# Kernel tuning notes

Measured on AMD Instinct MI355X. Metric: run time of the kernel, lower is better.

The kernel has to match this reference:

```python
import jax, jax.numpy as jnp
import numpy as np

N = 100000
F_IN = 512
HID = 256
C = 64
E = 3200000
K = 5


def _gcn_conv(h, W, b, src, dst, n):
    # h: [n, f_in] -> [n, f_out]; symmetric-normalized GCN with self-loops.
    hw = h @ W  # [n, f_out]
    loop = jnp.arange(n)
    s = jnp.concatenate([src, loop])
    d = jnp.concatenate([dst, loop])
    deg = jax.ops.segment_sum(jnp.ones_like(d, dtype=hw.dtype), d, num_segments=n)
    dinv = jnp.where(deg > 0, jax.lax.rsqrt(deg), 0.0)
    norm = dinv[s] * dinv[d]  # [E+n]
    out = jax.ops.segment_sum(norm[:, None] * hw[s], d, num_segments=n)
    return out + b


def _conv1d(x, w, b):
    # x: [1, C_in, L], w: [C_out, C_in, K], SAME padding (pad = (K-1)/2)
    y = jax.lax.conv_general_dilated(x, w, window_strides=(1,), padding='SAME',
                                     dimension_numbers=('NCW', 'OIW', 'NCW'))
    return y + b[None, :, None]


def setup_inputs() -> dict:
    key = jax.random.key(0)
    ks = jax.random.split(key, 16)

    def glorot(k, shape):
        fan_in, fan_out = shape[-2], shape[-1]
        lim = np.sqrt(6.0 / (fan_in + fan_out))
        return jax.random.uniform(k, shape, jnp.float32, -lim, lim)

    x = jax.random.normal(ks[0], (N, F_IN), jnp.float32)
    edge_index = jax.random.randint(ks[1], (2, E), 0, N, dtype=jnp.int64)

    W1 = glorot(ks[2], (F_IN, HID));  b1 = jnp.zeros((HID,), jnp.float32)
    W2 = glorot(ks[3], (HID, C));     b2 = jnp.zeros((C,), jnp.float32)
    Wp = glorot(ks[4], (C, 1));       bp = jnp.zeros((1,), jnp.float32)
    s1 = 1.0 / np.sqrt(C * K)
    cw1 = jax.random.uniform(ks[5], (C, C, K), jnp.float32, -s1, s1)
    cb1 = jax.random.uniform(ks[6], (C,), jnp.float32, -s1, s1)
    cw2 = jax.random.uniform(ks[7], (C, C, K), jnp.float32, -s1, s1)
    cb2 = jax.random.uniform(ks[8], (C,), jnp.float32, -s1, s1)
    Wl = glorot(ks[9], (2 * C, C));   bl = jnp.zeros((C,), jnp.float32)

    return {"x": x, "edge_index": edge_index, "W1": W1, "b1": b1, "W2": W2,
            "b2": b2, "Wp": Wp, "bp": bp, "cw1": cw1, "cb1": cb1,
            "cw2": cw2, "cb2": cb2, "Wl": Wl, "bl": bl}


def reference(x, edge_index, W1, b1, W2, b2, Wp, bp, cw1, cb1, cw2, cb2, Wl, bl):
    src, dst = edge_index[0], edge_index[1]
    n = x.shape[0]
    h = jax.nn.relu(_gcn_conv(x, W1, b1, src, dst, n))      # [N, HID]
    x1 = _gcn_conv(h, W2, b2, src, dst, n)                   # [N, C]

    g_score = x1 @ Wp + bp                                   # [N, 1]
    sort_idx = jnp.argsort(g_score[:, 0])                    # [N]
    inverse_idx = jnp.argsort(sort_idx)                      # [N]
    g_sorted = g_score[sort_idx]                             # [N, 1]
    sorted_x = g_sorted * x1[sort_idx]                       # [N, C]

    sx = sorted_x.T[None]                                    # [1, C, N]
    sx = jax.nn.relu(_conv1d(sx, cw1, cb1))
    sx = _conv1d(sx, cw2, cb2)
    sorted_out = sx[0].T                                     # [N, C]
    x2 = sorted_out[inverse_idx]                             # [N, C]

    out = jnp.concatenate([x1, x2], axis=1) @ Wl + bl        # [N, C]
    return jax.nn.log_softmax(out, axis=1)
```

## Files before the change

kernel.cpp:

```cpp
#include <hip/hip_runtime.h>
#include <cstdint>
#include <cstddef>

#define NF_IN 512
#define NHID 256
#define NC 64

typedef _Float16 f16x8 __attribute__((ext_vector_type(8)));
typedef float f32x4 __attribute__((ext_vector_type(4)));


__global__ void kb_hist(const int* __restrict__ dst, int e_total,
                        int* __restrict__ gh, int nbk){
  __shared__ int h[512];
  int t = threadIdx.x;
  for (int i=t;i<nbk;i+=256) h[i]=0;
  __syncthreads();
  int e0 = blockIdx.x*4096;
  #pragma unroll
  for (int j=0;j<16;j++){
    int e = e0 + j*256 + t;
    if (e < e_total) atomicAdd(&h[dst[e]>>8], 1);
  }
  __syncthreads();
  for (int i=t;i<nbk;i+=256) if (h[i]) atomicAdd(&gh[i], h[i]);
}

__global__ void k_scan1(int* __restrict__ data, int n){
  __shared__ int P[256];
  int t = threadIdx.x;
  int chunk = (n + 255) >> 8;
  int base = t*chunk;
  int s = 0;
  for (int j=0;j<chunk;j++) if (base+j<n) s += data[base+j];
  P[t]=s; __syncthreads();
  for (int o=1;o<256;o<<=1){
    int v = (t>=o)? P[t-o]:0; __syncthreads();
    P[t]+=v; __syncthreads();
  }
  int run = (t>0)? P[t-1] : 0;
  for (int j=0;j<chunk;j++) if (base+j<n){ int v = data[base+j]; data[base+j]=run; run+=v; }
}

__global__ void kb_copy(const int* __restrict__ a, int* __restrict__ b, int m){
  int i = blockIdx.x*256 + threadIdx.x;
  if (i < m) b[i] = a[i];
}

__global__ void kb_scatter(const int* __restrict__ src, const int* __restrict__ dst,
                           int e_total, int* __restrict__ bcur,
                           unsigned* __restrict__ pairs, int nbk){
  __shared__ int h[512];
  __shared__ int cb[512];
  int t = threadIdx.x;
  for (int i=t;i<nbk;i+=256) h[i]=0;
  __syncthreads();
  int e0 = blockIdx.x*4096;
  int d[16], s_[16];
  #pragma unroll
  for (int j=0;j<16;j++){
    int e = e0 + j*256 + t;
    if (e < e_total){ d[j]=dst[e]; s_[j]=src[e]; atomicAdd(&h[d[j]>>8],1); }
    else d[j] = -1;
  }
  __syncthreads();
  for (int i=t;i<nbk;i+=256){
    int c = h[i];
    cb[i] = c ? atomicAdd(&bcur[i], c) : 0;
    h[i] = 0;
  }
  __syncthreads();
  #pragma unroll
  for (int j=0;j<16;j++){
    if (d[j] >= 0){
      int bkt = d[j]>>8;
      int pos = cb[bkt] + atomicAdd(&h[bkt],1);
      pairs[pos] = ((unsigned)(d[j]&255)<<24) | (unsigned)s_[j];
    }
  }
}

__global__ __launch_bounds__(256) void kb_build(const unsigned* __restrict__ pairs,
    const int* __restrict__ bbase, int e_total, int nbk, int n,
    int* __restrict__ rowptr, int* __restrict__ cnt, float* __restrict__ dinv,
    int* __restrict__ csr){
  __shared__ int cL[256];
  __shared__ int sc[256];
  __shared__ int rpL[256];
  int b = blockIdx.x, t = threadIdx.x;
  int beg = bbase[b];
  int end = (b == nbk-1) ? e_total : bbase[b+1];
  cL[t] = 0; __syncthreads();
  for (int i=beg+t; i<end; i+=256) atomicAdd(&cL[pairs[i]>>24], 1);
  __syncthreads();
  int v = cL[t]; sc[t] = v; __syncthreads();
  for (int o=1;o<256;o<<=1){
    int w = (t>=o)? sc[t-o]:0; __syncthreads();
    sc[t] += w; __syncthreads();
  }
  rpL[t] = sc[t] - v;
  int node = b*256 + t;
  if (node < n){
    rowptr[node] = beg + rpL[t];
    cnt[node]    = v;
    dinv[node]   = 1.0f / sqrtf((float)(v + 1));
  }
  cL[t] = 0; __syncthreads();
  for (int i=beg+t; i<end; i+=256){
    unsigned p = pairs[i];
    int loc = p >> 24;
    int pos = beg + rpL[loc] + atomicAdd(&cL[loc], 1);
    csr[pos] = (int)(p & 0xFFFFFFu);
  }
}

__global__ __launch_bounds__(256) void k_sortnb(int* __restrict__ csr,
    const int* __restrict__ rowptr, const int* __restrict__ cnt, int n){
  int node = blockIdx.x*4 + (threadIdx.x>>6);
  int lane = threadIdx.x & 63;
  if (node >= n) return;
  int beg = rowptr[node], num = cnt[node];
  if (num <= 1 || num > 64) return;
  int v = (lane < num) ? csr[beg+lane] : 0x7fffffff;
  #pragma unroll
  for (int k=2; k<=64; k<<=1){
    for (int j=k>>1; j>0; j>>=1){
      int p = __shfl_xor(v, j);
      bool dirUp = ((lane & k) == 0);
      bool lower = ((lane & j) == 0);
      int mn = (v < p) ? v : p;
      int mx = (v < p) ? p : v;
      v = (dirUp == lower) ? mn : mx;
    }
  }
  if (lane < num) csr[beg+lane] = v;
}

__global__ void k_wsplit(const float* __restrict__ W, _Float16* __restrict__ WhT,
                         _Float16* __restrict__ WlT){
  int idx = blockIdx.x*256 + threadIdx.x;
  if (idx < NF_IN*NHID){
    int k = idx >> 8, nn = idx & 255;
    float w = W[idx];
    _Float16 h = (_Float16)w;
    _Float16 l = (_Float16)((w - (float)h) * 2048.0f);
    WhT[(size_t)nn*NF_IN + k] = h;
    WlT[(size_t)nn*NF_IN + k] = l;
  }
}

__global__ __launch_bounds__(512, 2) void k_mgemm1(
    const float* __restrict__ A, int lda,
    const _Float16* __restrict__ BhT, const _Float16* __restrict__ BlT, int ldb,
    float* __restrict__ C, int ldc, int M, int K, const float* __restrict__ dinv){
  __shared__ __align__(16) _Float16 Ah[128*40];
  __shared__ __align__(16) _Float16 Al[128*40];
  __shared__ __align__(16) _Float16 Bh[256*40];
  __shared__ __align__(16) _Float16 Bl[256*40];
  int t = threadIdx.x;
  int m0 = blockIdx.x*128;
  int wave = t>>6, lane = t&63;
  int wm = (wave>>2)*64, wn = (wave&3)*64;

  int arow = t>>2, akb = (t&3)*8;
  int ga = m0 + arow; if (ga >= M) ga = M - 1;
  const float* aptr = A + (size_t)ga*lda + akb;
  int brow = t>>1, bkb = (t&1)*16;
  const _Float16* bhp = BhT + (size_t)brow*ldb + bkb;
  const _Float16* blp = BlT + (size_t)brow*ldb + bkb;

  float4 a0 = *(const float4*)(aptr);
  float4 a1 = *(const float4*)(aptr+4);
  f16x8  b0 = *(const f16x8*)(bhp);
  f16x8  b1 = *(const f16x8*)(bhp+8);
  f16x8  c0 = *(const f16x8*)(blp);
  f16x8  c1 = *(const f16x8*)(blp+8);

  f32x4 acc1[4][4] = {};
  f32x4 acc2[4][4] = {};

  for (int k0 = 0; k0 < K; k0 += 32){
    __syncthreads();
    {
      float av[8] = {a0.x,a0.y,a0.z,a0.w, a1.x,a1.y,a1.z,a1.w};
      f16x8 h0, l0;
      #pragma unroll
      for (int j=0;j<8;j++){
        _Float16 hh = (_Float16)av[j];
        h0[j] = hh;
        l0[j] = (_Float16)((av[j] - (float)hh) * 2048.0f);
      }
      *(f16x8*)&Ah[arow*40+akb] = h0;
      *(f16x8*)&Al[arow*40+akb] = l0;
      *(f16x8*)&Bh[brow*40+bkb]   = b0;
      *(f16x8*)&Bh[brow*40+bkb+8] = b1;
      *(f16x8*)&Bl[brow*40+bkb]   = c0;
      *(f16x8*)&Bl[brow*40+bkb+8] = c1;
    }
    __syncthreads();
    if (k0 + 32 < K){
      a0 = *(const float4*)(aptr + k0+32);
      a1 = *(const float4*)(aptr + k0+36);
      b0 = *(const f16x8*)(bhp + k0+32);
      b1 = *(const f16x8*)(bhp + k0+40);
      c0 = *(const f16x8*)(blp + k0+32);
      c1 = *(const f16x8*)(blp + k0+40);
    }
    int fr = lane & 15, fk = (lane>>4)*8;
    f16x8 afh[4], afl[4];
    #pragma unroll
    for (int mf=0; mf<4; mf++){
      afh[mf] = *(const f16x8*)&Ah[(wm + mf*16 + fr)*40 + fk];
      afl[mf] = *(const f16x8*)&Al[(wm + mf*16 + fr)*40 + fk];
    }
    #pragma unroll
    for (int nf=0; nf<4; nf++){
      f16x8 bfh = *(const f16x8*)&Bh[(wn + nf*16 + fr)*40 + fk];
      f16x8 bfl = *(const f16x8*)&Bl[(wn + nf*16 + fr)*40 + fk];
      #pragma unroll
      for (int mf=0; mf<4; mf++){
        acc1[mf][nf] = __builtin_amdgcn_mfma_f32_16x16x32_f16(afh[mf], bfh, acc1[mf][nf], 0, 0, 0);
        acc2[mf][nf] = __builtin_amdgcn_mfma_f32_16x16x32_f16(afh[mf], bfl, acc2[mf][nf], 0, 0, 0);
        acc2[mf][nf] = __builtin_amdgcn_mfma_f32_16x16x32_f16(afl[mf], bfh, acc2[mf][nf], 0, 0, 0);
      }
    }
  }

  int fr = lane & 15, fq = lane >> 4;
  #pragma unroll
  for (int mf=0; mf<4; mf++){
    #pragma unroll
    for (int i=0;i<4;i++){
      int row = m0 + wm + mf*16 + fq*4 + i;
      if (row < M){
        float sc = dinv ? dinv[row] : 1.0f;
        #pragma unroll
        for (int nf=0; nf<4; nf++){
          float v = (acc1[mf][nf][i] + 0.00048828125f*acc2[mf][nf][i]) * sc;
          C[(size_t)row*ldc + wn + nf*16 + fr] = v;
        }
      }
    }
  }
}

__global__ __launch_bounds__(256) void k_gemm(const float* __restrict__ A, int lda,
    const float* __restrict__ B, int ldb, float* __restrict__ C, int ldc,
    int M, int K, const float* __restrict__ dinv){
  __shared__ float As[16*68];
  __shared__ float Bs[16*64];
  int t = threadIdx.x;
  int m0 = blockIdx.x*64, n0 = blockIdx.y*64;
  int tx = t & 15, ty = t >> 4;
  float acc[4][4] = {};
  int arow = m0 + (t>>2); if (arow >= M) arow = M-1;
  const float* aptr = A + (size_t)arow*lda + (t&3)*4;
  const float* bptr = B + (size_t)(t>>4)*ldb + n0 + (t&15)*4;
  for (int k0=0; k0<K; k0+=16){
    float4 av = *(const float4*)(aptr + k0);
    float4 bv = *(const float4*)(bptr + (size_t)k0*ldb);
    __syncthreads();
    int ak = (t&3)*4, ar = t>>2;
    As[(ak+0)*68 + ar] = av.x;
    As[(ak+1)*68 + ar] = av.y;
    As[(ak+2)*68 + ar] = av.z;
    As[(ak+3)*68 + ar] = av.w;
    *(float4*)&Bs[(t>>4)*64 + (t&15)*4] = bv;
    __syncthreads();
    #pragma unroll
    for (int kk=0;kk<16;kk++){
      float4 a4 = *(const float4*)&As[kk*68 + (ty<<2)];
      float4 b4 = *(const float4*)&Bs[(kk<<6) + (tx<<2)];
      float aa[4] = {a4.x,a4.y,a4.z,a4.w};
      float bb[4] = {b4.x,b4.y,b4.z,b4.w};
      #pragma unroll
      for (int i=0;i<4;i++)
        #pragma unroll
        for (int j=0;j<4;j++) acc[i][j] += aa[i]*bb[j];
    }
  }
  #pragma unroll
  for (int i=0;i<4;i++){
    int row = m0 + (ty<<2) + i;
    if (row < M){
      float sc = dinv ? dinv[row] : 1.0f;
      float4 vv; vv.x=acc[i][0]*sc; vv.y=acc[i][1]*sc; vv.z=acc[i][2]*sc; vv.w=acc[i][3]*sc;
      *(float4*)&C[(size_t)row*ldc + n0 + (tx<<2)] = vv;
    }
  }
}

__global__ __launch_bounds__(256, 4) void k_agg1(const float* __restrict__ u,
    const int* __restrict__ rowptr, const int* __restrict__ cnt,
    const int* __restrict__ csr, const float* __restrict__ dinv,
    const float* __restrict__ bias, float* __restrict__ outp, int n){
  int wid = blockIdx.x*4 + (threadIdx.x>>6);
  int lane = threadIdx.x & 63;
  if (wid >= n) return;
  const float4* up = (const float4*)u;
  float4 a = up[(size_t)wid*64 + lane];
  float ax=a.x, ay=a.y, az=a.z, aw=a.w;
  int beg = rowptr[wid], num = cnt[wid];
  int e = 0;
  int nb = num >> 4;
  if (nb > 0){
    int my = csr[beg + (lane & 15)];
    float4 v[8], w[8];
    #pragma unroll
    for (int q=0;q<8;q++){ int s = __shfl(my, q); v[q] = up[(size_t)s*64 + lane]; }
    int b = 0;
    for (;;){
      #pragma unroll
      for (int q=0;q<8;q++){ int s = __shfl(my, q+8); w[q] = up[(size_t)s*64 + lane]; }
      #pragma unroll
      for (int q=0;q<8;q++){ ax+=v[q].x; ay+=v[q].y; az+=v[q].z; aw+=v[q].w; }
      b++;
      if (b >= nb){
        #pragma unroll
        for (int q=0;q<8;q++){ ax+=w[q].x; ay+=w[q].y; az+=w[q].z; aw+=w[q].w; }
        break;
      }
      my = csr[beg + b*16 + (lane & 15)];
      #pragma unroll
      for (int q=0;q<8;q++){ int s = __shfl(my, q); v[q] = up[(size_t)s*64 + lane]; }
      #pragma unroll
      for (int q=0;q<8;q++){ ax+=w[q].x; ay+=w[q].y; az+=w[q].z; aw+=w[q].w; }
    }
    e = nb*16;
  }
  for (; e+4 <= num; e+=4){
    int my = csr[beg + e + (lane & 3)];
    float4 v[4];
    #pragma unroll
    for (int q=0;q<4;q++){ int s = __shfl(my, q); v[q] = up[(size_t)s*64 + lane]; }
    #pragma unroll
    for (int q=0;q<4;q++){ ax+=v[q].x; ay+=v[q].y; az+=v[q].z; aw+=v[q].w; }
  }
  for (; e<num; e++){
    int sN = csr[beg+e];
    float4 v = up[(size_t)sN*64 + lane];
    ax+=v.x; ay+=v.y; az+=v.z; aw+=v.w;
  }
  float di = dinv[wid];
  float4 b = ((const float4*)bias)[lane];
  float4 r;
  r.x = fmaxf(di*ax + b.x, 0.f);
  r.y = fmaxf(di*ay + b.y, 0.f);
  r.z = fmaxf(di*az + b.z, 0.f);
  r.w = fmaxf(di*aw + b.w, 0.f);
  ((float4*)outp)[(size_t)wid*64 + lane] = r;
}

__global__ __launch_bounds__(256) void k_agg2g(const float* __restrict__ u,
    const int* __restrict__ rowptr, const int* __restrict__ cnt,
    const int* __restrict__ csr, const float* __restrict__ dinv,
    const float* __restrict__ bias, float* __restrict__ outp, int n,
    const float* __restrict__ Wp, const float* __restrict__ bp,
    float* __restrict__ g, unsigned* __restrict__ keys, unsigned* __restrict__ vals){
  int wid = blockIdx.x*4 + (threadIdx.x>>6);
  int lane = threadIdx.x & 63;
  if (wid >= n) return;
  float acc = u[(size_t)wid*64 + lane];
  int beg = rowptr[wid], num = cnt[wid];
  int e = 0;
  for (; e+16 <= num; e+=16){
    int my = csr[beg + e + (lane & 15)];
    float v[16];
    #pragma unroll
    for (int q=0;q<16;q++){ int s = __shfl(my, q); v[q] = u[(size_t)s*64 + lane]; }
    #pragma unroll
    for (int q=0;q<16;q++) acc += v[q];
  }
  for (; e+4 <= num; e+=4){
    int my = csr[beg + e + (lane & 3)];
    float v[4];
    #pragma unroll
    for (int q=0;q<4;q++){ int s = __shfl(my, q); v[q] = u[(size_t)s*64 + lane]; }
    #pragma unroll
    for (int q=0;q<4;q++) acc += v[q];
  }
  for (; e<num; e++){
    int sN = csr[beg+e];
    acc += u[(size_t)sN*64 + lane];
  }
  float val = dinv[wid]*acc + bias[lane];
  outp[(size_t)wid*64 + lane] = val;
  float wv = val * Wp[lane];
  for (int o=32;o>0;o>>=1) wv += __shfl_xor(wv, o);
  if (lane == 0){
    float gg = wv + bp[0];
    g[wid] = gg;
    unsigned u_ = __float_as_uint(gg);
    u_ = (u_>>31) ? ~u_ : (u_ | 0x80000000u);
    keys[wid] = u_; vals[wid] = (unsigned)wid;
  }
}

__global__ void k_rhist(const unsigned* __restrict__ keys, int shift,
                        int* __restrict__ ghist, int n){
  __shared__ int h[16];
  int t = threadIdx.x;
  if (t < 16) h[t] = 0;
  __syncthreads();
  int base = blockIdx.x*1024 + t*4;
  #pragma unroll
  for (int j=0;j<4;j++)
    if (base+j < n){ int d = (keys[base+j]>>shift)&15; atomicAdd(&h[d],1); }
  __syncthreads();
  if (t < 16) ghist[t*gridDim.x + blockIdx.x] = h[t];
}

__global__ void k_rscatter(const unsigned* __restrict__ keys, const unsigned* __restrict__ vals,
                           int shift, const int* __restrict__ gbase,
                           unsigned* __restrict__ okeys, unsigned* __restrict__ ovals, int n){
  __shared__ int F[16*256];
  __shared__ int P[256];
  int t = threadIdx.x;
  int base = blockIdx.x*1024 + t*4;
  unsigned k[4]; int d[4];
  #pragma unroll
  for (int j=0;j<4;j++){
    bool ok = (base+j < n);
    k[j] = ok ? keys[base+j] : 0u;
    d[j] = (int)((k[j]>>shift)&15u);
    if (!ok) d[j] = -1;
  }
  #pragma unroll
  for (int dig=0;dig<16;dig++){
    int c = 0;
    #pragma unroll
    for (int j=0;j<4;j++) if (d[j]==dig) c++;
    F[dig*256 + t] = c;
  }
  __syncthreads();
  int loc[16]; int s = 0;
  #pragma unroll
  for (int q=0;q<16;q++){ loc[q] = F[t*16+q]; s += loc[q]; }
  P[t] = s; __syncthreads();
  for (int o=1;o<256;o<<=1){
    int v = (t>=o)? P[t-o]:0; __syncthreads();
    P[t] += v; __syncthreads();
  }
  int run = (t>0)? P[t-1] : 0;
  #pragma unroll
  for (int q=0;q<16;q++){ F[t*16+q] = run; run += loc[q]; }
  __syncthreads();
  #pragma unroll
  for (int j=0;j<4;j++){
    if (base+j < n){
      int dd = d[j];
      int r = 0;
      #pragma unroll
      for (int jj=0;jj<4;jj++) if (jj<j && d[jj]==dd) r++;
      int pos = gbase[dd*gridDim.x + blockIdx.x] + (F[dd*256 + t] - F[dd*256]) + r;
      okeys[pos] = k[j];
      ovals[pos] = vals[base+j];
    }
  }
}

__global__ void k_ssx(const unsigned* __restrict__ sidx, const float* __restrict__ g,
                      const float* __restrict__ x1, float* __restrict__ ssx,
                      int* __restrict__ inv, int n){
  int idx = blockIdx.x*256 + threadIdx.x;
  if (idx < n*64){
    int p = idx>>6, c = idx&63;
    int j = (int)sidx[p];
    ssx[idx] = g[j] * x1[(size_t)j*64 + c];
    if (c==0) inv[j] = p;
  }
}

__global__ void k_wt(const float* __restrict__ cw1, const float* __restrict__ cw2,
                     float* __restrict__ wT1, float* __restrict__ wT2){
  int idx = blockIdx.x*256 + threadIdx.x;
  if (idx < 2*20480){
    const float* s = (idx < 20480) ? cw1 : cw2;
    float* o = (idx < 20480) ? wT1 : wT2;
    int i = idx % 20480;
    int kk = i % 5, ci = (i/5) % 64, co = i / 320;
    o[((kk<<6)+ci)*64 + co] = s[i];
  }
}

__global__ __launch_bounds__(256) void k_conv(const float* __restrict__ inp,
    const float* __restrict__ wT, const float* __restrict__ bias,
    float* __restrict__ outp, int n, int do_relu){
  __shared__ float xin[132*65];
  int t = threadIdx.x;
  int r0 = blockIdx.x*128;
  for (int idx=t; idx<132*64; idx+=256){
    int r = idx>>6, c = idx&63;
    int gr = r0 + r - 2;
    xin[r*65 + c] = (gr>=0 && gr<n) ? inp[(size_t)gr*64 + c] : 0.f;
  }
  __syncthreads();
  int rg = t & 15, cg = t >> 4;
  float acc[8][4] = {};
  for (int k=0;k<5;k++){
    for (int ci=0;ci<64;ci++){
      float4 w = *(const float4*)&wT[((k<<6)+ci)*64 + (cg<<2)];
      #pragma unroll
      for (int rr=0;rr<8;rr++){
        float xv = xin[(rg + (rr<<4) + k)*65 + ci];
        acc[rr][0] += xv*w.x; acc[rr][1] += xv*w.y;
        acc[rr][2] += xv*w.z; acc[rr][3] += xv*w.w;
      }
    }
  }
  float4 b = ((const float4*)bias)[cg];
  #pragma unroll
  for (int rr=0;rr<8;rr++){
    int row = r0 + rg + (rr<<4);
    if (row < n){
      float4 v;
      v.x = acc[rr][0]+b.x; v.y = acc[rr][1]+b.y; v.z = acc[rr][2]+b.z; v.w = acc[rr][3]+b.w;
      if (do_relu){ v.x=fmaxf(v.x,0.f); v.y=fmaxf(v.y,0.f); v.z=fmaxf(v.z,0.f); v.w=fmaxf(v.w,0.f); }
      *(float4*)&outp[(size_t)row*64 + (cg<<2)] = v;
    }
  }
}

__global__ __launch_bounds__(256) void k_fgemm(const float* __restrict__ x1,
    const float* __restrict__ y2, const int* __restrict__ inv,
    const float* __restrict__ Wl, const float* __restrict__ bl,
    float* __restrict__ outp, int M){
  __shared__ float As[16*68];
  __shared__ float Bs[16*64];
  __shared__ float Pr[64*16];
  __shared__ float Ms[64];
  __shared__ float Ls[64];
  int t = threadIdx.x;
  int m0 = blockIdx.x*64;
  int tx = t & 15, ty = t >> 4;
  float acc[4][4] = {};
  int arow = m0 + (t>>2); if (arow >= M) arow = M-1;
  int acol0 = (t&3)*4;
  int invr = inv[arow];
  const float* bptr = Wl + (size_t)(t>>4)*64 + tx*4;
  for (int k0=0; k0<128; k0+=16){
    int acol = acol0 + k0;
    float4 av = (acol < 64) ? *(const float4*)&x1[(size_t)arow*64 + acol]
                            : *(const float4*)&y2[(size_t)invr*64 + (acol-64)];
    float4 bv = *(const float4*)(bptr + (size_t)k0*64);
    __syncthreads();
    int ak = (t&3)*4, ar = t>>2;
    As[(ak+0)*68 + ar] = av.x;
    As[(ak+1)*68 + ar] = av.y;
    As[(ak+2)*68 + ar] = av.z;
    As[(ak+3)*68 + ar] = av.w;
    *(float4*)&Bs[(t>>4)*64 + (t&15)*4] = bv;
    __syncthreads();
    #pragma unroll
    for (int kk=0;kk<16;kk++){
      float4 a4 = *(const float4*)&As[kk*68 + (ty<<2)];
      float4 b4 = *(const float4*)&Bs[(kk<<6) + (tx<<2)];
      float aa[4] = {a4.x,a4.y,a4.z,a4.w};
      float bb[4] = {b4.x,b4.y,b4.z,b4.w};
      #pragma unroll
      for (int i=0;i<4;i++)
        #pragma unroll
        for (int j=0;j<4;j++) acc[i][j] += aa[i]*bb[j];
    }
  }
  float v[4][4];
  #pragma unroll
  for (int i=0;i<4;i++)
    #pragma unroll
    for (int j=0;j<4;j++) v[i][j] = acc[i][j] + bl[(tx<<2)+j];
  #pragma unroll
  for (int i=0;i<4;i++){
    float pm = fmaxf(fmaxf(v[i][0],v[i][1]), fmaxf(v[i][2],v[i][3]));
    Pr[((ty<<2)+i)*16 + tx] = pm;
  }
  __syncthreads();
  if (t < 64){
    float m = Pr[t*16];
    #pragma unroll
    for (int k=1;k<16;k++) m = fmaxf(m, Pr[t*16+k]);
    Ms[t] = m;
  }
  __syncthreads();
  #pragma unroll
  for (int i=0;i<4;i++){
    float m = Ms[(ty<<2)+i];
    float ps = expf(v[i][0]-m)+expf(v[i][1]-m)+expf(v[i][2]-m)+expf(v[i][3]-m);
    Pr[((ty<<2)+i)*16 + tx] = ps;
  }
  __syncthreads();
  if (t < 64){
    float s = 0.f;
    #pragma unroll
    for (int k=0;k<16;k++) s += Pr[t*16+k];
    Ls[t] = logf(s);
  }
  __syncthreads();
  #pragma unroll
  for (int i=0;i<4;i++){
    int row = m0 + (ty<<2) + i;
    if (row < M){
      float m = Ms[(ty<<2)+i], l = Ls[(ty<<2)+i];
      float4 o;
      o.x = v[i][0]-m-l; o.y = v[i][1]-m-l; o.z = v[i][2]-m-l; o.w = v[i][3]-m-l;
      *(float4*)&outp[(size_t)row*64 + (tx<<2)] = o;
    }
  }
}

extern "C" void kernel_launch(void* const* d_in, const int* in_sizes, int n_in,
                              void* d_out, int out_size, void* d_ws, size_t ws_size,
                              hipStream_t stream) {
  const float* x   = (const float*)d_in[0];
  const int*   ei  = (const int*)d_in[1];
  const float* W1  = (const float*)d_in[2];
  const float* b1  = (const float*)d_in[3];
  const float* W2  = (const float*)d_in[4];
  const float* b2  = (const float*)d_in[5];
  const float* Wp  = (const float*)d_in[6];
  const float* bp  = (const float*)d_in[7];
  const float* cw1 = (const float*)d_in[8];
  const float* cb1 = (const float*)d_in[9];
  const float* cw2 = (const float*)d_in[10];
  const float* cb2 = (const float*)d_in[11];
  const float* Wl  = (const float*)d_in[12];
  const float* bl  = (const float*)d_in[13];
  float* out = (float*)d_out;

  const int n = in_sizes[0] / NF_IN;
  const int e_total = in_sizes[1] / 2;
  const int* srcp = ei;
  const int* dstp = ei + e_total;

  char* ws = (char*)d_ws;
  size_t off = 0;
  auto take = [&](size_t bytes)->char* {
    char* p = ws + off; off = (off + bytes + 255) & ~(size_t)255; return p;
  };
  const int NB  = (n + 1023) / 1024;
  const int NBK = (n + 255) >> 8;
  const int NEB = (e_total + 4095) / 4096;
  int*      cnt    = (int*)     take((size_t)n*4);
  int*      rowptr = (int*)     take((size_t)n*4);
  float*    dinv   = (float*)   take((size_t)n*4);
  float*    g      = (float*)   take((size_t)n*4);
  int*      inv    = (int*)     take((size_t)n*4);
  unsigned* keys0  = (unsigned*)take((size_t)n*4);
  unsigned* vals0  = (unsigned*)take((size_t)n*4);
  unsigned* keys1  = (unsigned*)take((size_t)n*4);
  unsigned* vals1  = (unsigned*)take((size_t)n*4);
  int*      ghist  = (int*)     take((size_t)(16*NB)*4);
  int*      bh     = (int*)     take(512*4);
  int*      bcur   = (int*)     take(512*4);
  int*      csr    = (int*)     take((size_t)e_total*4);
  float*    wT1    = (float*)   take(20480*4);
  float*    wT2    = (float*)   take(20480*4);
  _Float16* w1h    = (_Float16*)take((size_t)NF_IN*NHID*2);
  _Float16* w1l    = (_Float16*)take((size_t)NF_IN*NHID*2);
  float*    bigA   = (float*)   take((size_t)n*256*4);
  float*    bigB   = (float*)   take((size_t)n*256*4);
  unsigned* pairs  = (unsigned*)bigA;
  float* u1  = bigA;
  float* h   = bigB;
  float* u2  = bigA;
  float* x1  = bigA + (size_t)n*64;
  float* ssx = bigA + (size_t)n*128;
  float* y1  = bigA + (size_t)n*192;
  float* y2  = bigB;

  const int nb128 = (n + 127) / 128;
  const int nb64  = (n + 63) / 64;
  const int nbAgg = (n + 3) / 4;

  hipMemsetAsync(bh, 0, (size_t)NBK*4, stream);
  kb_hist<<<NEB, 256, 0, stream>>>(dstp, e_total, bh, NBK);
  k_scan1<<<1, 256, 0, stream>>>(bh, NBK);
  kb_copy<<<(NBK+255)/256, 256, 0, stream>>>(bh, bcur, NBK);
  kb_scatter<<<NEB, 256, 0, stream>>>(srcp, dstp, e_total, bcur, pairs, NBK);
  kb_build<<<NBK, 256, 0, stream>>>(pairs, bh, e_total, NBK, n, rowptr, cnt, dinv, csr);
  k_sortnb<<<nbAgg, 256, 0, stream>>>(csr, rowptr, cnt, n);

  k_wsplit<<<(NF_IN*NHID+255)/256, 256, 0, stream>>>(W1, w1h, w1l);
  k_mgemm1<<<dim3(nb128, 1), 512, 0, stream>>>(x, NF_IN, w1h, w1l, NF_IN, u1, NHID, n, NF_IN, dinv);
  k_agg1<<<nbAgg, 256, 0, stream>>>(u1, rowptr, cnt, csr, dinv, b1, h, n);

  k_gemm<<<dim3(nb64, 1), 256, 0, stream>>>(h, NHID, W2, NC, u2, NC, n, NHID, dinv);
  k_agg2g<<<nbAgg, 256, 0, stream>>>(u2, rowptr, cnt, csr, dinv, b2, x1, n,
                                     Wp, bp, g, keys0, vals0);

  unsigned *ka = keys0, *va = vals0, *kb = keys1, *vb = vals1;
  for (int p = 0; p < 8; p++){
    k_rhist<<<NB, 256, 0, stream>>>(ka, p*4, ghist, n);
    k_scan1<<<1, 256, 0, stream>>>(ghist, 16*NB);
    k_rscatter<<<NB, 256, 0, stream>>>(ka, va, p*4, ghist, kb, vb, n);
    unsigned* tk = ka; ka = kb; kb = tk;
    unsigned* tv = va; va = vb; vb = tv;
  }

  k_ssx<<<(n*64+255)/256, 256, 0, stream>>>(va, g, x1, ssx, inv, n);

  k_wt<<<(2*20480+255)/256, 256, 0, stream>>>(cw1, cw2, wT1, wT2);
  k_conv<<<(n+127)/128, 256, 0, stream>>>(ssx, wT1, cb1, y1, n, 1);
  k_conv<<<(n+127)/128, 256, 0, stream>>>(y1, wT2, cb2, y2, n, 0);

  k_fgemm<<<nb64, 256, 0, stream>>>(x1, y2, inv, Wl, bl, out, n);
}
```

Before: 1.461 ms.

## Switch radix sort to 8-bit digits with ballot ranking and fused next-pass histogram

Replaces the eight 4-bit radix passes with four 8-bit passes. Ranking within a block now uses wave ballots, and each scatter also builds the next pass's histogram with global atomics, so the separate histogram kernels go away. The scan plus copy of the bucket offsets is merged into one kernel. The per-node neighbour bitonic sort is removed, which changes CSR neighbour order and therefore the floating-point summation order. In exchange, the single-block scan now covers 256*NB entries, and the fused histogram adds global atomic traffic and memsets.

```diff
diff --git a/kernel.cpp b/kernel.cpp
--- a/kernel.cpp
+++ b/kernel.cpp
@@ -8,7 +8,6 @@
 
 typedef _Float16 f16x8 __attribute__((ext_vector_type(8)));
 typedef float f32x4 __attribute__((ext_vector_type(4)));
-
 
 __global__ void kb_hist(const int* __restrict__ dst, int e_total,
                         int* __restrict__ gh, int nbk){
@@ -42,9 +41,20 @@
   for (int j=0;j<chunk;j++) if (base+j<n){ int v = data[base+j]; data[base+j]=run; run+=v; }
 }
 
-__global__ void kb_copy(const int* __restrict__ a, int* __restrict__ b, int m){
-  int i = blockIdx.x*256 + threadIdx.x;
-  if (i < m) b[i] = a[i];
+__global__ void kb_scan1c(int* __restrict__ data, int* __restrict__ cpy, int n){
+  __shared__ int P[256];
+  int t = threadIdx.x;
+  int chunk = (n + 255) >> 8;
+  int base = t*chunk;
+  int s = 0;
+  for (int j=0;j<chunk;j++) if (base+j<n) s += data[base+j];
+  P[t]=s; __syncthreads();
+  for (int o=1;o<256;o<<=1){
+    int v = (t>=o)? P[t-o]:0; __syncthreads();
+    P[t]+=v; __syncthreads();
+  }
+  int run = (t>0)? P[t-1] : 0;
+  for (int j=0;j<chunk;j++) if (base+j<n){ int v = data[base+j]; data[base+j]=run; cpy[base+j]=run; run+=v; }
 }
 
 __global__ void kb_scatter(const int* __restrict__ src, const int* __restrict__ dst,
@@ -112,28 +122,6 @@
     int pos = beg + rpL[loc] + atomicAdd(&cL[loc], 1);
     csr[pos] = (int)(p & 0xFFFFFFu);
   }
-}
-
-__global__ __launch_bounds__(256) void k_sortnb(int* __restrict__ csr,
-    const int* __restrict__ rowptr, const int* __restrict__ cnt, int n){
-  int node = blockIdx.x*4 + (threadIdx.x>>6);
-  int lane = threadIdx.x & 63;
-  if (node >= n) return;
-  int beg = rowptr[node], num = cnt[node];
-  if (num <= 1 || num > 64) return;
-  int v = (lane < num) ? csr[beg+lane] : 0x7fffffff;
-  #pragma unroll
-  for (int k=2; k<=64; k<<=1){
-    for (int j=k>>1; j>0; j>>=1){
-      int p = __shfl_xor(v, j);
-      bool dirUp = ((lane & k) == 0);
-      bool lower = ((lane & j) == 0);
-      int mn = (v < p) ? v : p;
-      int mx = (v < p) ? p : v;
-      v = (dirUp == lower) ? mn : mx;
-    }
-  }
-  if (lane < num) csr[beg+lane] = v;
 }
 
 __global__ void k_wsplit(const float* __restrict__ W, _Float16* __restrict__ WhT,
@@ -396,65 +384,88 @@
   }
 }
 
-__global__ void k_rhist(const unsigned* __restrict__ keys, int shift,
-                        int* __restrict__ ghist, int n){
-  __shared__ int h[16];
-  int t = threadIdx.x;
-  if (t < 16) h[t] = 0;
+__global__ void k_rhist8(const unsigned* __restrict__ keys, int shift,
+                         int* __restrict__ gh, int n, int nb){
+  __shared__ int h[256];
+  int t = threadIdx.x;
+  h[t] = 0;
   __syncthreads();
   int base = blockIdx.x*1024 + t*4;
   #pragma unroll
   for (int j=0;j<4;j++)
-    if (base+j < n){ int d = (keys[base+j]>>shift)&15; atomicAdd(&h[d],1); }
-  __syncthreads();
-  if (t < 16) ghist[t*gridDim.x + blockIdx.x] = h[t];
-}
-
-__global__ void k_rscatter(const unsigned* __restrict__ keys, const unsigned* __restrict__ vals,
-                           int shift, const int* __restrict__ gbase,
-                           unsigned* __restrict__ okeys, unsigned* __restrict__ ovals, int n){
-  __shared__ int F[16*256];
-  __shared__ int P[256];
-  int t = threadIdx.x;
+    if (base+j < n) atomicAdd(&h[(keys[base+j]>>shift)&255], 1);
+  __syncthreads();
+  gh[t*nb + blockIdx.x] = h[t];
+}
+
+__global__ __launch_bounds__(256) void k_rscat8(
+    const unsigned* __restrict__ keys, const unsigned* __restrict__ vals,
+    int shift, const int* __restrict__ gbase, int nb,
+    unsigned* __restrict__ okeys, unsigned* __restrict__ ovals,
+    int* __restrict__ gh_next, int next_shift, int n){
+  __shared__ int whist[4][256];
+  __shared__ int wbase[4][256];
+  int t = threadIdx.x;
+  int w = t>>6, lane = t&63;
+  #pragma unroll
+  for (int q=0;q<4;q++) whist[q][t] = 0;
+  __syncthreads();
   int base = blockIdx.x*1024 + t*4;
-  unsigned k[4]; int d[4];
+  unsigned k[4], v[4]; int d[4]; bool ok[4];
   #pragma unroll
   for (int j=0;j<4;j++){
-    bool ok = (base+j < n);
-    k[j] = ok ? keys[base+j] : 0u;
-    d[j] = (int)((k[j]>>shift)&15u);
-    if (!ok) d[j] = -1;
-  }
-  #pragma unroll
-  for (int dig=0;dig<16;dig++){
-    int c = 0;
-    #pragma unroll
-    for (int j=0;j<4;j++) if (d[j]==dig) c++;
-    F[dig*256 + t] = c;
-  }
-  __syncthreads();
-  int loc[16]; int s = 0;
-  #pragma unroll
-  for (int q=0;q<16;q++){ loc[q] = F[t*16+q]; s += loc[q]; }
-  P[t] = s; __syncthreads();
-  for (int o=1;o<256;o<<=1){
-    int v = (t>=o)? P[t-o]:0; __syncthreads();
-    P[t] += v; __syncthreads();
-  }
-  int run = (t>0)? P[t-1] : 0;
-  #pragma unroll
-  for (int q=0;q<16;q++){ F[t*16+q] = run; run += loc[q]; }
-  __syncthreads();
+    ok[j] = (base+j < n);
+    k[j] = ok[j] ? keys[base+j] : 0u;
+    v[j] = ok[j] ? vals[base+j] : 0u;
+    d[j] = (int)((k[j]>>shift)&255u);
+    if (ok[j]) atomicAdd(&whist[w][d[j]], 1);
+  }
+  __syncthreads();
+  {
+    int c0=whist[0][t], c1=whist[1][t], c2=whist[2][t];
+    wbase[0][t]=0; wbase[1][t]=c0; wbase[2][t]=c0+c1; wbase[3][t]=c0+c1+c2;
+  }
+  __syncthreads();
+  int rank[4] = {0,0,0,0};
+  unsigned long long below = (lane==0)? 0ull : ((~0ull) >> (64-lane));
+  unsigned long long self  = 1ull << lane;
+  #pragma unroll
+  for (int jp=0; jp<4; jp++){
+    unsigned long long B0 = __ballot((d[jp]>>0)&1);
+    unsigned long long B1 = __ballot((d[jp]>>1)&1);
+    unsigned long long B2 = __ballot((d[jp]>>2)&1);
+    unsigned long long B3 = __ballot((d[jp]>>3)&1);
+    unsigned long long B4 = __ballot((d[jp]>>4)&1);
+    unsigned long long B5 = __ballot((d[jp]>>5)&1);
+    unsigned long long B6 = __ballot((d[jp]>>6)&1);
+    unsigned long long B7 = __ballot((d[jp]>>7)&1);
+    unsigned long long Vb = __ballot(ok[jp]);
+    #pragma unroll
+    for (int j=0;j<4;j++){
+      unsigned long long m = Vb;
+      m &= ((d[j]>>0)&1) ? B0 : ~B0;
+      m &= ((d[j]>>1)&1) ? B1 : ~B1;
+      m &= ((d[j]>>2)&1) ? B2 : ~B2;
+      m &= ((d[j]>>3)&1) ? B3 : ~B3;
+      m &= ((d[j]>>4)&1) ? B4 : ~B4;
+      m &= ((d[j]>>5)&1) ? B5 : ~B5;
+      m &= ((d[j]>>6)&1) ? B6 : ~B6;
+      m &= ((d[j]>>7)&1) ? B7 : ~B7;
+      unsigned long long sel = (jp < j) ? (below | self) : below;
+      rank[j] += __popcll(m & sel);
+    }
+  }
   #pragma unroll
   for (int j=0;j<4;j++){
-    if (base+j < n){
+    if (ok[j]){
       int dd = d[j];
-      int r = 0;
-      #pragma unroll
-      for (int jj=0;jj<4;jj++) if (jj<j && d[jj]==dd) r++;
-      int pos = gbase[dd*gridDim.x + blockIdx.x] + (F[dd*256 + t] - F[dd*256]) + r;
+      int pos = gbase[dd*nb + blockIdx.x] + wbase[w][dd] + rank[j];
       okeys[pos] = k[j];
-      ovals[pos] = vals[base+j];
+      ovals[pos] = v[j];
+      if (gh_next){
+        int nd = (int)((k[j]>>next_shift)&255u);
+        atomicAdd(&gh_next[nd*nb + (pos>>10)], 1);
+      }
     }
   }
 }
@@ -648,7 +659,8 @@
   unsigned* vals0  = (unsigned*)take((size_t)n*4);
   unsigned* keys1  = (unsigned*)take((size_t)n*4);
   unsigned* vals1  = (unsigned*)take((size_t)n*4);
-  int*      ghist  = (int*)     take((size_t)(16*NB)*4);
+  int*      ghA    = (int*)     take((size_t)(256*NB)*4);
+  int*      ghB    = (int*)     take((size_t)(256*NB)*4);
   int*      bh     = (int*)     take(512*4);
   int*      bcur   = (int*)     take(512*4);
   int*      csr    = (int*)     take((size_t)e_total*4);
@@ -673,11 +685,9 @@
 
   hipMemsetAsync(bh, 0, (size_t)NBK*4, stream);
   kb_hist<<<NEB, 256, 0, stream>>>(dstp, e_total, bh, NBK);
-  k_scan1<<<1, 256, 0, stream>>>(bh, NBK);
-  kb_copy<<<(NBK+255)/256, 256, 0, stream>>>(bh, bcur, NBK);
+  kb_scan1c<<<1, 256, 0, stream>>>(bh, bcur, NBK);
   kb_scatter<<<NEB, 256, 0, stream>>>(srcp, dstp, e_total, bcur, pairs, NBK);
   kb_build<<<NBK, 256, 0, stream>>>(pairs, bh, e_total, NBK, n, rowptr, cnt, dinv, csr);
-  k_sortnb<<<nbAgg, 256, 0, stream>>>(csr, rowptr, cnt, n);
 
   k_wsplit<<<(NF_IN*NHID+255)/256, 256, 0, stream>>>(W1, w1h, w1l);
   k_mgemm1<<<dim3(nb128, 1), 512, 0, stream>>>(x, NF_IN, w1h, w1l, NF_IN, u1, NHID, n, NF_IN, dinv);
@@ -687,16 +697,21 @@
   k_agg2g<<<nbAgg, 256, 0, stream>>>(u2, rowptr, cnt, csr, dinv, b2, x1, n,
                                      Wp, bp, g, keys0, vals0);
 
-  unsigned *ka = keys0, *va = vals0, *kb = keys1, *vb = vals1;
-  for (int p = 0; p < 8; p++){
-    k_rhist<<<NB, 256, 0, stream>>>(ka, p*4, ghist, n);
-    k_scan1<<<1, 256, 0, stream>>>(ghist, 16*NB);
-    k_rscatter<<<NB, 256, 0, stream>>>(ka, va, p*4, ghist, kb, vb, n);
-    unsigned* tk = ka; ka = kb; kb = tk;
-    unsigned* tv = va; va = vb; vb = tv;
-  }
-
-  k_ssx<<<(n*64+255)/256, 256, 0, stream>>>(va, g, x1, ssx, inv, n);
+  {
+    unsigned *ka = keys0, *va = vals0, *kb = keys1, *vb = vals1;
+    int *gcur = ghA, *gnext = ghB;
+    k_rhist8<<<NB, 256, 0, stream>>>(ka, 0, gcur, n, NB);
+    for (int p = 0; p < 4; p++){
+      if (p < 3) hipMemsetAsync(gnext, 0, (size_t)(256*NB)*4, stream);
+      k_scan1<<<1, 256, 0, stream>>>(gcur, 256*NB);
+      k_rscat8<<<NB, 256, 0, stream>>>(ka, va, p*8, gcur, NB, kb, vb,
+                                       (p<3)? gnext : nullptr, (p<3)? (p+1)*8 : 0, n);
+      unsigned* tk = ka; ka = kb; kb = tk;
+      unsigned* tv = va; va = vb; vb = tv;
+      int* tg = gcur; gcur = gnext; gnext = tg;
+    }
+    k_ssx<<<(n*64+255)/256, 256, 0, stream>>>(va, g, x1, ssx, inv, n);
+  }
 
   k_wt<<<(2*20480+255)/256, 256, 0, stream>>>(cw1, cw2, wT1, wT2);
   k_conv<<<(n+127)/128, 256, 0, stream>>>(ssx, wT1, cb1, y1, n, 1);
```

Measured after the change: 1.624 ms. 11.2% more time.

## Fuse layer-1 aggregation with W2 GEMM and drop neighbor sort and copy kernel

Applied to the files above, without the earlier changes.

The layer-1 aggregation now also does the 256x64 W2 projection from LDS in a persistent 512-block kernel. This removes the h intermediate (N x 256 floats) write and read-back and the separate GEMM launch. It also deletes the per-node neighbor bitonic sort and folds the bucket copy into the scan. Without the sort, gather order within a row changes and the sums may differ slightly. The 64KB W2 tile in LDS plus a scalar dot-product loop may limit occupancy and compute throughput.

```diff
diff --git a/kernel.cpp b/kernel.cpp
--- a/kernel.cpp
+++ b/kernel.cpp
@@ -8,7 +8,6 @@
 
 typedef _Float16 f16x8 __attribute__((ext_vector_type(8)));
 typedef float f32x4 __attribute__((ext_vector_type(4)));
-
 
 __global__ void kb_hist(const int* __restrict__ dst, int e_total,
                         int* __restrict__ gh, int nbk){
@@ -42,9 +41,20 @@
   for (int j=0;j<chunk;j++) if (base+j<n){ int v = data[base+j]; data[base+j]=run; run+=v; }
 }
 
-__global__ void kb_copy(const int* __restrict__ a, int* __restrict__ b, int m){
-  int i = blockIdx.x*256 + threadIdx.x;
-  if (i < m) b[i] = a[i];
+__global__ void kb_scan1c(int* __restrict__ data, int* __restrict__ cpy, int n){
+  __shared__ int P[256];
+  int t = threadIdx.x;
+  int chunk = (n + 255) >> 8;
+  int base = t*chunk;
+  int s = 0;
+  for (int j=0;j<chunk;j++) if (base+j<n) s += data[base+j];
+  P[t]=s; __syncthreads();
+  for (int o=1;o<256;o<<=1){
+    int v = (t>=o)? P[t-o]:0; __syncthreads();
+    P[t]+=v; __syncthreads();
+  }
+  int run = (t>0)? P[t-1] : 0;
+  for (int j=0;j<chunk;j++) if (base+j<n){ int v = data[base+j]; data[base+j]=run; cpy[base+j]=run; run+=v; }
 }
 
 __global__ void kb_scatter(const int* __restrict__ src, const int* __restrict__ dst,
@@ -114,28 +124,6 @@
   }
 }
 
-__global__ __launch_bounds__(256) void k_sortnb(int* __restrict__ csr,
-    const int* __restrict__ rowptr, const int* __restrict__ cnt, int n){
-  int node = blockIdx.x*4 + (threadIdx.x>>6);
-  int lane = threadIdx.x & 63;
-  if (node >= n) return;
-  int beg = rowptr[node], num = cnt[node];
-  if (num <= 1 || num > 64) return;
-  int v = (lane < num) ? csr[beg+lane] : 0x7fffffff;
-  #pragma unroll
-  for (int k=2; k<=64; k<<=1){
-    for (int j=k>>1; j>0; j>>=1){
-      int p = __shfl_xor(v, j);
-      bool dirUp = ((lane & k) == 0);
-      bool lower = ((lane & j) == 0);
-      int mn = (v < p) ? v : p;
-      int mx = (v < p) ? p : v;
-      v = (dirUp == lower) ? mn : mx;
-    }
-  }
-  if (lane < num) csr[beg+lane] = v;
-}
-
 __global__ void k_wsplit(const float* __restrict__ W, _Float16* __restrict__ WhT,
                          _Float16* __restrict__ WlT){
   int idx = blockIdx.x*256 + threadIdx.x;
@@ -244,111 +232,78 @@
   }
 }
 
-__global__ __launch_bounds__(256) void k_gemm(const float* __restrict__ A, int lda,
-    const float* __restrict__ B, int ldb, float* __restrict__ C, int ldc,
-    int M, int K, const float* __restrict__ dinv){
-  __shared__ float As[16*68];
-  __shared__ float Bs[16*64];
-  int t = threadIdx.x;
-  int m0 = blockIdx.x*64, n0 = blockIdx.y*64;
-  int tx = t & 15, ty = t >> 4;
-  float acc[4][4] = {};
-  int arow = m0 + (t>>2); if (arow >= M) arow = M-1;
-  const float* aptr = A + (size_t)arow*lda + (t&3)*4;
-  const float* bptr = B + (size_t)(t>>4)*ldb + n0 + (t&15)*4;
-  for (int k0=0; k0<K; k0+=16){
-    float4 av = *(const float4*)(aptr + k0);
-    float4 bv = *(const float4*)(bptr + (size_t)k0*ldb);
-    __syncthreads();
-    int ak = (t&3)*4, ar = t>>2;
-    As[(ak+0)*68 + ar] = av.x;
-    As[(ak+1)*68 + ar] = av.y;
-    As[(ak+2)*68 + ar] = av.z;
-    As[(ak+3)*68 + ar] = av.w;
-    *(float4*)&Bs[(t>>4)*64 + (t&15)*4] = bv;
-    __syncthreads();
-    #pragma unroll
-    for (int kk=0;kk<16;kk++){
-      float4 a4 = *(const float4*)&As[kk*68 + (ty<<2)];
-      float4 b4 = *(const float4*)&Bs[(kk<<6) + (tx<<2)];
-      float aa[4] = {a4.x,a4.y,a4.z,a4.w};
-      float bb[4] = {b4.x,b4.y,b4.z,b4.w};
-      #pragma unroll
-      for (int i=0;i<4;i++)
-        #pragma unroll
-        for (int j=0;j<4;j++) acc[i][j] += aa[i]*bb[j];
-    }
-  }
-  #pragma unroll
-  for (int i=0;i<4;i++){
-    int row = m0 + (ty<<2) + i;
-    if (row < M){
-      float sc = dinv ? dinv[row] : 1.0f;
-      float4 vv; vv.x=acc[i][0]*sc; vv.y=acc[i][1]*sc; vv.z=acc[i][2]*sc; vv.w=acc[i][3]*sc;
-      *(float4*)&C[(size_t)row*ldc + n0 + (tx<<2)] = vv;
-    }
-  }
-}
-
-__global__ __launch_bounds__(256, 4) void k_agg1(const float* __restrict__ u,
+__global__ __launch_bounds__(512, 4) void k_agg1f(const float* __restrict__ u,
     const int* __restrict__ rowptr, const int* __restrict__ cnt,
     const int* __restrict__ csr, const float* __restrict__ dinv,
-    const float* __restrict__ bias, float* __restrict__ outp, int n){
-  int wid = blockIdx.x*4 + (threadIdx.x>>6);
-  int lane = threadIdx.x & 63;
-  if (wid >= n) return;
+    const float* __restrict__ bias, const float* __restrict__ W2,
+    float* __restrict__ u2, int n){
+  __shared__ float W2s[256*64];
+  __shared__ float hL[8][256];
+  int t = threadIdx.x;
+  for (int i=t; i<256*64; i+=512) W2s[i] = W2[i];
+  __syncthreads();
+  int wave = t>>6, lane = t&63;
   const float4* up = (const float4*)u;
-  float4 a = up[(size_t)wid*64 + lane];
-  float ax=a.x, ay=a.y, az=a.z, aw=a.w;
-  int beg = rowptr[wid], num = cnt[wid];
-  int e = 0;
-  int nb = num >> 4;
-  if (nb > 0){
-    int my = csr[beg + (lane & 15)];
-    float4 v[8], w[8];
-    #pragma unroll
-    for (int q=0;q<8;q++){ int s = __shfl(my, q); v[q] = up[(size_t)s*64 + lane]; }
-    int b = 0;
-    for (;;){
-      #pragma unroll
-      for (int q=0;q<8;q++){ int s = __shfl(my, q+8); w[q] = up[(size_t)s*64 + lane]; }
-      #pragma unroll
-      for (int q=0;q<8;q++){ ax+=v[q].x; ay+=v[q].y; az+=v[q].z; aw+=v[q].w; }
-      b++;
-      if (b >= nb){
+  int ngrp = (n + 7) >> 3;
+  for (int grp = blockIdx.x; grp < ngrp; grp += gridDim.x){
+    int wid = grp*8 + wave;
+    if (wid >= n) continue;
+    float4 a = up[(size_t)wid*64 + lane];
+    float ax=a.x, ay=a.y, az=a.z, aw=a.w;
+    int beg = rowptr[wid], num = cnt[wid];
+    int e = 0;
+    int nb = num >> 4;
+    if (nb > 0){
+      int my = csr[beg + (lane & 15)];
+      float4 v[8], w[8];
+      #pragma unroll
+      for (int q=0;q<8;q++){ int s = __shfl(my, q); v[q] = up[(size_t)s*64 + lane]; }
+      int b = 0;
+      for (;;){
+        #pragma unroll
+        for (int q=0;q<8;q++){ int s = __shfl(my, q+8); w[q] = up[(size_t)s*64 + lane]; }
+        #pragma unroll
+        for (int q=0;q<8;q++){ ax+=v[q].x; ay+=v[q].y; az+=v[q].z; aw+=v[q].w; }
+        b++;
+        if (b >= nb){
+          #pragma unroll
+          for (int q=0;q<8;q++){ ax+=w[q].x; ay+=w[q].y; az+=w[q].z; aw+=w[q].w; }
+          break;
+        }
+        my = csr[beg + b*16 + (lane & 15)];
+        #pragma unroll
+        for (int q=0;q<8;q++){ int s = __shfl(my, q); v[q] = up[(size_t)s*64 + lane]; }
         #pragma unroll
         for (int q=0;q<8;q++){ ax+=w[q].x; ay+=w[q].y; az+=w[q].z; aw+=w[q].w; }
-        break;
       }
-      my = csr[beg + b*16 + (lane & 15)];
-      #pragma unroll
-      for (int q=0;q<8;q++){ int s = __shfl(my, q); v[q] = up[(size_t)s*64 + lane]; }
-      #pragma unroll
-      for (int q=0;q<8;q++){ ax+=w[q].x; ay+=w[q].y; az+=w[q].z; aw+=w[q].w; }
-    }
-    e = nb*16;
-  }
-  for (; e+4 <= num; e+=4){
-    int my = csr[beg + e + (lane & 3)];
-    float4 v[4];
-    #pragma unroll
-    for (int q=0;q<4;q++){ int s = __shfl(my, q); v[q] = up[(size_t)s*64 + lane]; }
-    #pragma unroll
-    for (int q=0;q<4;q++){ ax+=v[q].x; ay+=v[q].y; az+=v[q].z; aw+=v[q].w; }
-  }
-  for (; e<num; e++){
-    int sN = csr[beg+e];
-    float4 v = up[(size_t)sN*64 + lane];
-    ax+=v.x; ay+=v.y; az+=v.z; aw+=v.w;
-  }
-  float di = dinv[wid];
-  float4 b = ((const float4*)bias)[lane];
-  float4 r;
-  r.x = fmaxf(di*ax + b.x, 0.f);
-  r.y = fmaxf(di*ay + b.y, 0.f);
-  r.z = fmaxf(di*az + b.z, 0.f);
-  r.w = fmaxf(di*aw + b.w, 0.f);
-  ((float4*)outp)[(size_t)wid*64 + lane] = r;
+      e = nb*16;
+    }
+    for (; e+4 <= num; e+=4){
+      int my = csr[beg + e + (lane & 3)];
+      float4 v[4];
+      #pragma unroll
+      for (int q=0;q<4;q++){ int s = __shfl(my, q); v[q] = up[(size_t)s*64 + lane]; }
+      #pragma unroll
+      for (int q=0;q<4;q++){ ax+=v[q].x; ay+=v[q].y; az+=v[q].z; aw+=v[q].w; }
+    }
+    for (; e<num; e++){
+      int sN = csr[beg+e];
+      float4 v = up[(size_t)sN*64 + lane];
+      ax+=v.x; ay+=v.y; az+=v.z; aw+=v.w;
+    }
+    float di = dinv[wid];
+    float4 b = ((const float4*)bias)[lane];
+    float4 hv;
+    hv.x = fmaxf(di*ax + b.x, 0.f);
+    hv.y = fmaxf(di*ay + b.y, 0.f);
+    hv.z = fmaxf(di*az + b.z, 0.f);
+    hv.w = fmaxf(di*aw + b.w, 0.f);
+    ((float4*)hL[wave])[lane] = hv;
+    float acc = 0.f;
+    #pragma unroll 8
+    for (int c=0;c<256;c++) acc += hL[wave][c] * W2s[(c<<6) + lane];
+    u2[(size_t)wid*64 + lane] = di * acc;
+  }
 }
 
 __global__ __launch_bounds__(256) void k_agg2g(const float* __restrict__ u,
@@ -660,12 +615,11 @@
   float*    bigB   = (float*)   take((size_t)n*256*4);
   unsigned* pairs  = (unsigned*)bigA;
   float* u1  = bigA;
-  float* h   = bigB;
-  float* u2  = bigA;
   float* x1  = bigA + (size_t)n*64;
   float* ssx = bigA + (size_t)n*128;
   float* y1  = bigA + (size_t)n*192;
-  float* y2  = bigB;
+  float* u2  = bigB;
+  float* y2  = bigB + (size_t)n*64;
 
   const int nb128 = (n + 127) / 128;
   const int nb64  = (n + 63) / 64;
@@ -673,17 +627,15 @@
 
   hipMemsetAsync(bh, 0, (size_t)NBK*4, stream);
   kb_hist<<<NEB, 256, 0, stream>>>(dstp, e_total, bh, NBK);
-  k_scan1<<<1, 256, 0, stream>>>(bh, NBK);
-  kb_copy<<<(NBK+255)/256, 256, 0, stream>>>(bh, bcur, NBK);
+  kb_scan1c<<<1, 256, 0, stream>>>(bh, bcur, NBK);
   kb_scatter<<<NEB, 256, 0, stream>>>(srcp, dstp, e_total, bcur, pairs, NBK);
   kb_build<<<NBK, 256, 0, stream>>>(pairs, bh, e_total, NBK, n, rowptr, cnt, dinv, csr);
-  k_sortnb<<<nbAgg, 256, 0, stream>>>(csr, rowptr, cnt, n);
 
   k_wsplit<<<(NF_IN*NHID+255)/256, 256, 0, stream>>>(W1, w1h, w1l);
   k_mgemm1<<<dim3(nb128, 1), 512, 0, stream>>>(x, NF_IN, w1h, w1l, NF_IN, u1, NHID, n, NF_IN, dinv);
-  k_agg1<<<nbAgg, 256, 0, stream>>>(u1, rowptr, cnt, csr, dinv, b1, h, n);
-
-  k_gemm<<<dim3(nb64, 1), 256, 0, stream>>>(h, NHID, W2, NC, u2, NC, n, NHID, dinv);
+
+  k_agg1f<<<512, 512, 0, stream>>>(u1, rowptr, cnt, csr, dinv, b1, W2, u2, n);
+
   k_agg2g<<<nbAgg, 256, 0, stream>>>(u2, rowptr, cnt, csr, dinv, b2, x1, n,
                                      Wp, bp, g, keys0, vals0);
 
```

New measurement: 1.374 ms. 5.9% less time.
